# Kernel optimization log

Measured on AMD Instinct MI355X. Metric: run time of the kernel, lower is better.

## Reference

```python
import jax, jax.numpy as jnp
import numpy as np

L, B, T, D, H, F, V = 8, 2, 1024, 1024, 16, 4096, 50257


def _ln(x, w, b):
    m = jnp.mean(x, axis=-1, keepdims=True)
    v = jnp.mean((x - m) ** 2, axis=-1, keepdims=True)
    return (x - m) * jax.lax.rsqrt(v + 1e-5) * w + b


def setup_inputs() -> dict:
    key = jax.random.key(0)
    ks = iter(jax.random.split(key, 16))
    s = jnp.float32(0.02)
    w = lambda shape: jax.random.normal(next(ks), shape, jnp.float32) * s
    return {
        'idx': jax.random.randint(next(ks), (B, T), 0, V, jnp.int32),
        'emb': w((V, D)),
        'pos_emb': w((T, D)),
        'ln1_w': jnp.ones((L, D), jnp.float32),
        'ln1_b': jnp.zeros((L, D), jnp.float32),
        'qkv_w': w((L, D, 3 * D)),
        'qkv_b': jnp.zeros((L, 3 * D), jnp.float32),
        'ln2_w': jnp.ones((L, D), jnp.float32),
        'ln2_b': jnp.zeros((L, D), jnp.float32),
        'fc1_w': w((L, D, F)),
        'fc1_b': jnp.zeros((L, F), jnp.float32),
        'fc2_w': w((L, F, D)),
        'fc2_b': jnp.zeros((L, D), jnp.float32),
        'lnf_w': jnp.ones((D,), jnp.float32),
        'lnf_b': jnp.zeros((D,), jnp.float32),
        'head_w': w((D, V)),
        'head_b': jnp.zeros((V,), jnp.float32),
    }


def reference(idx, emb, pos_emb, ln1_w, ln1_b, qkv_w, qkv_b, ln2_w, ln2_b,
              fc1_w, fc1_b, fc2_w, fc2_b, lnf_w, lnf_b, head_w, head_b):
    b, t = idx.shape
    d = emb.shape[1]
    hd = d // H
    x = emb[idx] + pos_emb[:t]                      # [b,t,d]
    mask = jnp.tril(jnp.ones((t, t), bool))         # causal mask
    inv_scale = jnp.float32(1.0 / (d ** 0.5))       # NOTE: source scales by sqrt(full dim), not head_dim

    def layer(x, p):
        l1w, l1b, qw, qb, l2w, l2b, f1w, f1b, f2w, f2b = p
        h = _ln(x, l1w, l1b)
        qkv = h @ qw + qb                           # [b,t,3d]
        q, k, v = jnp.split(qkv, 3, axis=-1)
        q = q.reshape(b, t, H, hd)
        k = k.reshape(b, t, H, hd)
        v = v.reshape(b, t, H, hd)
        logits = jnp.einsum('bqhe,bkhe->bhqk', q, k) * inv_scale
        logits = jnp.where(mask, logits, -jnp.inf)
        attn = jax.nn.softmax(logits, axis=-1)
        o = jnp.einsum('bhqk,bkhe->bqhe', attn, v).reshape(b, t, d)
        x = x + o                                   # no output projection in source
        h = _ln(x, l2w, l2b)
        h = jax.nn.gelu(h @ f1w + f1b, approximate=False)
        h = jax.nn.gelu(h @ f2w + f2b, approximate=False)  # GELU after fc2 too, per source
        return x + h, None

    x, _ = jax.lax.scan(
        layer, x,
        (ln1_w, ln1_b, qkv_w, qkv_b, ln2_w, ln2_b, fc1_w, fc1_b, fc2_w, fc2_b))
    x = _ln(x, lnf_w, lnf_b)
    return x @ head_w + head_b                      # [b,t,V] logits
```

## Files before the change

kernel.cpp:

```cpp
#include <hip/hip_runtime.h>
#include <math.h>

#define Ln 8
#define Bn 2
#define Tn 1024
#define Dm 1024
#define Hn 16
#define Fm 4096
#define Vn 50257
#define NTOK 2048

typedef unsigned short u16;
typedef u16   u16x8  __attribute__((ext_vector_type(8)));
typedef __bf16 bf16x8 __attribute__((ext_vector_type(8)));
typedef float f32x4  __attribute__((ext_vector_type(4)));

__device__ __forceinline__ u16 f2bf(float f){
  unsigned u = __builtin_bit_cast(unsigned, f);
  u += 0x7FFFu + ((u >> 16) & 1u);
  return (u16)(u >> 16);
}
__device__ __forceinline__ float bf2f(u16 s){
  return __builtin_bit_cast(float, ((unsigned)s) << 16);
}
__device__ __forceinline__ float gelu_f(float v){
  return 0.5f * v * (1.0f + erff(v * 0.70710678118654752440f));
}
__device__ __forceinline__ void gload16(const void* g, void* l){
  __builtin_amdgcn_global_load_lds(
      (const __attribute__((address_space(1))) void*)g,
      (__attribute__((address_space(3))) void*)l, 16, 0, 0);
}

__global__ __launch_bounds__(256) void embed_kernel(const int* __restrict__ idx,
                                                    const float* __restrict__ emb,
                                                    const float* __restrict__ pos,
                                                    float* __restrict__ x){
  int row = blockIdx.x;
  int t = row & (Tn - 1);
  int id = idx[row];
  const float4* e = (const float4*)(emb + (size_t)id * Dm);
  const float4* p = (const float4*)(pos + (size_t)t * Dm);
  float4* o = (float4*)(x + (size_t)row * Dm);
  int i = threadIdx.x;
  float4 a = e[i], b = p[i];
  o[i] = make_float4(a.x + b.x, a.y + b.y, a.z + b.z, a.w + b.w);
}

__global__ __launch_bounds__(256) void ln_kernel(const float* __restrict__ xin,
                                                 const float* __restrict__ w,
                                                 const float* __restrict__ bb,
                                                 u16* __restrict__ out){
  int row = blockIdx.x;
  int t = threadIdx.x;
  float4 v = ((const float4*)(xin + (size_t)row * Dm))[t];
  float s  = v.x + v.y + v.z + v.w;
  float s2 = v.x*v.x + v.y*v.y + v.z*v.z + v.w*v.w;
  #pragma unroll
  for (int off = 1; off < 64; off <<= 1){
    s  += __shfl_xor(s, off);
    s2 += __shfl_xor(s2, off);
  }
  __shared__ float red[8];
  int wv = t >> 6, lane = t & 63;
  if (lane == 0){ red[wv] = s; red[4 + wv] = s2; }
  __syncthreads();
  s  = red[0] + red[1] + red[2] + red[3];
  s2 = red[4] + red[5] + red[6] + red[7];
  float mean = s * (1.0f / Dm);
  float var  = s2 * (1.0f / Dm) - mean * mean;
  float rs = rsqrtf(var + 1e-5f);
  float4 wv4 = ((const float4*)w)[t];
  float4 bv4 = ((const float4*)bb)[t];
  u16 o4[4];
  o4[0] = f2bf((v.x - mean) * rs * wv4.x + bv4.x);
  o4[1] = f2bf((v.y - mean) * rs * wv4.y + bv4.y);
  o4[2] = f2bf((v.z - mean) * rs * wv4.z + bv4.z);
  o4[3] = f2bf((v.w - mean) * rs * wv4.w + bv4.w);
  *(uint2*)(out + (size_t)row * Dm + t * 4) = *(uint2*)o4;
}

__device__ __forceinline__ void trans_tile(const float* __restrict__ src,
                                           u16* __restrict__ dst,
                                           int N, int K, int srcCol, int dstRow, int k0){
  __shared__ float tile[64][66];
  int t = threadIdx.x;
  int rr = t >> 4, nc = (t & 15) * 4;
  #pragma unroll
  for (int u = 0; u < 4; u++){
    int kk = rr + u * 16;
    int gn = srcCol + nc;
    const float* sp = src + (size_t)(k0 + kk) * N;
    float4 v;
    if (gn + 3 < N) v = *(const float4*)(sp + gn);
    else {
      v.x = (gn     < N) ? sp[gn]     : 0.0f;
      v.y = (gn + 1 < N) ? sp[gn + 1] : 0.0f;
      v.z = (gn + 2 < N) ? sp[gn + 2] : 0.0f;
      v.w = (gn + 3 < N) ? sp[gn + 3] : 0.0f;
    }
    tile[kk][nc]     = v.x;
    tile[kk][nc + 1] = v.y;
    tile[kk][nc + 2] = v.z;
    tile[kk][nc + 3] = v.w;
  }
  __syncthreads();
  int np = t >> 2, c = t & 3;
  u16* dp = dst + (size_t)(dstRow + np) * K + k0;
  u16 pk[8];
  #pragma unroll
  for (int j = 0; j < 8; j++) pk[j] = f2bf(tile[c*8 + j][np]);
  *(int4*)(dp + c*8) = *(int4*)pk;
  #pragma unroll
  for (int j = 0; j < 8; j++) pk[j] = f2bf(tile[32 + c*8 + j][np]);
  *(int4*)(dp + 32 + c*8) = *(int4*)pk;
}

__global__ __launch_bounds__(256) void transpose_w(const float* __restrict__ Bw,
                                                   u16* __restrict__ Bt,
                                                   int N, int K, int c0){
  int n0 = blockIdx.x * 64, k0 = blockIdx.y * 64;
  trans_tile(Bw, Bt, N, K, c0 + n0, n0, k0);
}

__global__ __launch_bounds__(256) void mega_transpose(const float* __restrict__ qkvw,
                                                      const float* __restrict__ fc1w,
                                                      const float* __restrict__ fc2w,
                                                      const float* __restrict__ headw,
                                                      u16* __restrict__ Wq,
                                                      u16* __restrict__ W1,
                                                      u16* __restrict__ W2,
                                                      u16* __restrict__ Wh){
  int id = blockIdx.x;
  const float* src; u16* dst; int N, K, n0, k0;
  if (id < 6144){
    int l = id / 768, r = id % 768;
    n0 = (r % 48) * 64; k0 = (r / 48) * 64;
    src = qkvw + (size_t)l * Dm * 3072; dst = Wq + (size_t)l * 3072 * Dm;
    N = 3072; K = Dm;
  } else if (id < 14336){
    int id2 = id - 6144;
    int l = id2 / 1024, r = id2 % 1024;
    n0 = (r % 64) * 64; k0 = (r / 64) * 64;
    src = fc1w + (size_t)l * Dm * Fm; dst = W1 + (size_t)l * Fm * Dm;
    N = Fm; K = Dm;
  } else if (id < 22528){
    int id2 = id - 14336;
    int l = id2 / 1024, r = id2 % 1024;
    n0 = (r % 16) * 64; k0 = (r / 16) * 64;
    src = fc2w + (size_t)l * Fm * Dm; dst = W2 + (size_t)l * Dm * Fm;
    N = Dm; K = Fm;
  } else {
    int id2 = id - 22528;
    n0 = (id2 % 788) * 64; k0 = (id2 / 788) * 64;
    src = headw; dst = Wh;
    N = Vn; K = Dm;
  }
  trans_tile(src, dst, N, K, n0, n0, k0);
}

template<int MODE, int BMt, int BNt, int WM, int WN, bool SWZ>
__global__ __launch_bounds__(256) void gemm_kernel(const u16* __restrict__ A,
                                                   const u16* __restrict__ Bt,
                                                   const float* __restrict__ bias,
                                                   void* __restrict__ outp,
                                                   float* __restrict__ resid,
                                                   u16* __restrict__ vT,
                                                   int K, int Nout, int c0){
  constexpr int MR = BMt / (WM * 16);
  constexpr int NR = BNt / (WN * 16);
  __shared__ u16 sA[BMt][64];
  __shared__ u16 sB[BNt][64];
  int t = threadIdx.x;
  int lane = t & 63, w = t >> 6;
  int wm = w / WN, wn = w % WN;
  int lr = lane & 15, lg = lane >> 4;
  int m0, n0;
  if (SWZ){
    int orig = blockIdx.x;
    int q = gridDim.x >> 3;
    int wg = (orig & 7) * q + (orig >> 3);
    m0 = (wg & 15) * BMt;
    n0 = (wg >> 4) * BNt;
  } else {
    m0 = blockIdx.y * BMt; n0 = blockIdx.x * BNt;
  }

  f32x4 acc[MR][NR] = {};

  int srow = lane >> 3;
  int gcs = ((lane & 7) ^ (lane >> 3)) * 8;
  int cswz = (lr & 7) << 3;

  for (int k0 = 0; k0 < K; k0 += 64){
    __syncthreads();
    #pragma unroll
    for (int i = 0; i < BMt/32; i++){
      int rbase = i*32 + w*8;
      gload16(A + (size_t)(m0 + rbase + srow) * K + k0 + gcs, (char*)&sA[rbase][0]);
    }
    #pragma unroll
    for (int i = 0; i < BNt/32; i++){
      int rbase = i*32 + w*8;
      gload16(Bt + (size_t)(n0 + rbase + srow) * K + k0 + gcs, (char*)&sB[rbase][0]);
    }
    __syncthreads();
    #pragma unroll
    for (int kk = 0; kk < 2; kk++){
      bf16x8 af[MR], bfr[NR];
      #pragma unroll
      for (int i = 0; i < MR; i++) af[i]  = *(const bf16x8*)&sA[wm*(MR*16) + i*16 + lr][(kk*32 + lg*8) ^ cswz];
      #pragma unroll
      for (int j = 0; j < NR; j++) bfr[j] = *(const bf16x8*)&sB[wn*(NR*16) + j*16 + lr][(kk*32 + lg*8) ^ cswz];
      #pragma unroll
      for (int i = 0; i < MR; i++)
        #pragma unroll
        for (int j = 0; j < NR; j++)
          acc[i][j] = __builtin_amdgcn_mfma_f32_16x16x32_bf16(af[i], bfr[j], acc[i][j], 0, 0, 0);
    }
  }

  #pragma unroll
  for (int i = 0; i < MR; i++){
    int gr0 = m0 + wm*(MR*16) + i*16 + lg*4;
    #pragma unroll
    for (int j = 0; j < NR; j++){
      int gc = c0 + n0 + wn*(NR*16) + j*16 + lr;
      if (MODE == 3 && gc >= Nout) continue;
      float bb = bias[gc];
      if (MODE == 0 && gc >= 2048){
        int hh = (gc - 2048) >> 6, dd = (gc - 2048) & 63;
        int b_ = gr0 >> 10, tt = gr0 & 1023;
        u16 pk[4];
        #pragma unroll
        for (int r = 0; r < 4; r++) pk[r] = f2bf(acc[i][j][r] + bb);
        *(uint2*)&vT[((size_t)((b_*Hn + hh)*64 + dd))*Tn + tt] = *(uint2*)pk;
        continue;
      }
      #pragma unroll
      for (int r = 0; r < 4; r++){
        float v = acc[i][j][r] + bb;
        size_t oi = (size_t)(gr0 + r) * Nout + gc;
        if (MODE == 0)      ((u16*)outp)[oi] = f2bf(v);
        else if (MODE == 1) ((u16*)outp)[oi] = f2bf(gelu_f(v));
        else if (MODE == 2) resid[oi] = resid[oi] + gelu_f(v);
        else                ((float*)outp)[oi] = v;
      }
    }
  }
}

#define BARR() __builtin_amdgcn_s_barrier()
#define LGK0() asm volatile("s_waitcnt lgkmcnt(0)" ::: "memory")
#define VMC4() asm volatile("s_waitcnt vmcnt(4)" ::: "memory")

__global__ __launch_bounds__(512) void head_gemm_8ph(const u16* __restrict__ A,
                                                     const u16* __restrict__ Bw,
                                                     const float* __restrict__ bias,
                                                     float* __restrict__ out){
  __shared__ u16 sA[2][256][64];
  __shared__ u16 sB[2][256][64];
  int t = threadIdx.x, lane = t & 63, w = t >> 6;
  int wm = w >> 2, wn = w & 3;
  int lr = lane & 15, lg = lane >> 4;
  int orig = blockIdx.x;
  int wg = (orig & 7) * (gridDim.x >> 3) + (orig >> 3);
  int m0g = (wg & 7) << 8;
  int n0g = (wg >> 3) << 8;

  int srow = w*8 + (lane >> 3);
  int scol = ((lane & 7) ^ (lane >> 3)) * 8;
  const u16* Abase = A  + (size_t)(m0g + srow) * 1024 + scol;
  const u16* Bbase = Bw + (size_t)(n0g + srow) * 1024 + scol;

  f32x4 acc[8][4] = {};
  bf16x8 a[4][2], b0[2][2], b1[2][2];
  int rsw = (lr & 7) << 3;

  auto stA = [&](int buf, int half, int tile){
    const u16* s = Abase + (size_t)half*128*1024 + tile*64;
    gload16(s,           &sA[buf][half*128 +      w*8][0]);
    gload16(s + 64*1024, &sA[buf][half*128 + 64 + w*8][0]);
  };
  auto stB = [&](int buf, int half, int tile){
    const u16* s = Bbase + (size_t)half*128*1024 + tile*64;
    gload16(s,           &sB[buf][half*128 +      w*8][0]);
    gload16(s + 64*1024, &sB[buf][half*128 + 64 + w*8][0]);
  };
  auto rdA = [&](int buf, int half){
    #pragma unroll
    for (int i = 0; i < 4; i++)
      #pragma unroll
      for (int kk = 0; kk < 2; kk++)
        a[i][kk] = *(const bf16x8*)&sA[buf][wm*128 + half*64 + i*16 + lr][(kk*32 + lg*8) ^ rsw];
  };
  auto rdB = [&](int buf, int half, bf16x8 (&bb)[2][2]){
    #pragma unroll
    for (int j = 0; j < 2; j++)
      #pragma unroll
      for (int kk = 0; kk < 2; kk++)
        bb[j][kk] = *(const bf16x8*)&sB[buf][wn*64 + half*32 + j*16 + lr][(kk*32 + lg*8) ^ rsw];
  };
  auto MF = [&](int mb, int nb, bf16x8 (&bb)[2][2]){
    __builtin_amdgcn_s_setprio(1);
    #pragma unroll
    for (int kk = 0; kk < 2; kk++)
      #pragma unroll
      for (int i = 0; i < 4; i++)
        #pragma unroll
        for (int j = 0; j < 2; j++)
          acc[mb+i][nb+j] = __builtin_amdgcn_mfma_f32_16x16x32_bf16(a[i][kk], bb[j][kk], acc[mb+i][nb+j], 0, 0, 0);
    __builtin_amdgcn_s_setprio(0);
  };

  stA(0,0,0); stA(0,1,0); stB(0,0,0); stB(0,1,0);
  stB(1,0,1); stB(1,1,1);
  VMC4();
  BARR();

  for (int it = 0; it < 8; ++it){
    int T = it * 2;
    rdA(0,0); rdB(0,0,b0);
    stA(1,0,T+1);
    BARR(); LGK0(); MF(0,0,b0); BARR();
    rdB(0,1,b1);
    stA(1,1,T+1);
    BARR(); LGK0(); MF(0,2,b1); BARR();
    rdA(0,1);
    if (T+2 < 16) stB(0,0,T+2);
    BARR(); LGK0(); MF(4,2,b1); BARR();
    if (T+2 < 16) stB(0,1,T+2);
    BARR(); MF(4,0,b0); VMC4(); BARR();
    rdA(1,0); rdB(1,0,b0);
    if (T+2 < 16) stA(0,0,T+2);
    BARR(); LGK0(); MF(0,0,b0); BARR();
    rdB(1,1,b1);
    if (T+2 < 16) stA(0,1,T+2);
    BARR(); LGK0(); MF(0,2,b1); BARR();
    rdA(1,1);
    if (T+3 < 16) stB(1,0,T+3);
    BARR(); LGK0(); MF(4,2,b1); BARR();
    if (T+3 < 16) stB(1,1,T+3);
    BARR(); MF(4,0,b0); VMC4(); BARR();
  }

  #pragma unroll
  for (int m = 0; m < 8; m++){
    int gr = m0g + wm*128 + m*16 + lg*4;
    #pragma unroll
    for (int n = 0; n < 4; n++){
      int gc = n0g + wn*64 + n*16 + lr;
      if (gc < Vn){
        float bb = bias[gc];
        #pragma unroll
        for (int r = 0; r < 4; r++)
          out[(size_t)(gr + r) * Vn + gc] = acc[m][n][r] + bb;
      }
    }
  }
}

__global__ __launch_bounds__(256) void attn_mfma(const u16* __restrict__ qkv,
                                                 const u16* __restrict__ vT,
                                                 float* __restrict__ x){
  int bid = blockIdx.x;
  int bh = bid & 31;
  int j = bid >> 5;
  int qt = (j < 8) ? (15 - j) : (j - 8);
  int b = bh >> 4, h_ = bh & 15;
  int t = threadIdx.x;
  int w = t >> 6, lane = t & 63;
  int lr = lane & 15, lg = lane >> 4;

  __shared__ u16 sK [2][64][72];
  __shared__ u16 sVt[2][64][72];
  __shared__ u16 sP [64][72];

  const u16* qbase = qkv + ((size_t)(b*Tn + qt*64 + w*16 + lr)) * 3*Dm + h_*64 + lg*8;
  bf16x8 qf[2];
  #pragma unroll
  for (int i = 0; i < 2; i++){
    u16x8 raw = *(const u16x8*)(qbase + i * 32);
    #pragma unroll
    for (int u = 0; u < 8; u++) qf[i][u] = (__bf16)(bf2f(raw[u]) * 0.03125f);
  }

  f32x4 o_[4] = {};
  float m_[4], l_[4];
  #pragma unroll
  for (int r = 0; r < 4; r++){ m_[r] = -INFINITY; l_[r] = 0.0f; }

  int sr = t >> 2, scc = (t & 3) * 16;
  const u16* kbase = qkv + ((size_t)(b*Tn + sr)) * 3*Dm + Dm + h_*64 + scc;
  const u16* vbase = vT + ((size_t)(bh*64 + sr)) * Tn + scc;
  int4 kr0, kr1, vr0, vr1;

  kr0 = *(const int4*)(kbase);     kr1 = *(const int4*)(kbase + 8);
  vr0 = *(const int4*)(vbase);     vr1 = *(const int4*)(vbase + 8);
  *(int4*)&sK [0][sr][scc]     = kr0;  *(int4*)&sK [0][sr][scc + 8] = kr1;
  *(int4*)&sVt[0][sr][scc]     = vr0;  *(int4*)&sVt[0][sr][scc + 8] = vr1;

  for (int kt = 0; kt <= qt; kt++){
    int cur = kt & 1;
    if (kt < qt){
      const u16* kb = kbase + (size_t)(kt + 1) * 64 * 3 * Dm;
      const u16* vb = vbase + (kt + 1) * 64;
      kr0 = *(const int4*)(kb);    kr1 = *(const int4*)(kb + 8);
      vr0 = *(const int4*)(vb);    vr1 = *(const int4*)(vb + 8);
    }
    __syncthreads();

    f32x4 s[4] = {};
    __builtin_amdgcn_s_setprio(1);
    #pragma unroll
    for (int kf = 0; kf < 2; kf++){
      #pragma unroll
      for (int nf = 0; nf < 4; nf++){
        bf16x8 kfrag = *(const bf16x8*)&sK[cur][nf*16 + lr][kf*32 + lg*8];
        s[nf] = __builtin_amdgcn_mfma_f32_16x16x32_bf16(qf[kf], kfrag, s[nf], 0, 0, 0);
      }
    }
    __builtin_amdgcn_s_setprio(0);

    bool lastt = (kt == qt);
    float tmax[4] = {-INFINITY, -INFINITY, -INFINITY, -INFINITY};
    #pragma unroll
    for (int nf = 0; nf < 4; nf++)
      #pragma unroll
      for (int r = 0; r < 4; r++){
        float v = s[nf][r];
        if (lastt){
          int kkg = nf*16 + lr, qg = w*16 + lg*4 + r;
          if (kkg > qg) v = -INFINITY;
        }
        s[nf][r] = v;
        tmax[r] = fmaxf(tmax[r], v);
      }
    #pragma unroll
    for (int r = 0; r < 4; r++){
      tmax[r] = fmaxf(tmax[r], __shfl_xor(tmax[r], 1));
      tmax[r] = fmaxf(tmax[r], __shfl_xor(tmax[r], 2));
      tmax[r] = fmaxf(tmax[r], __shfl_xor(tmax[r], 4));
      tmax[r] = fmaxf(tmax[r], __shfl_xor(tmax[r], 8));
    }
    bool need = false;
    #pragma unroll
    for (int r = 0; r < 4; r++) need = need || (tmax[r] > m_[r] + 8.0f);
    if (__any(need)){
      #pragma unroll
      for (int r = 0; r < 4; r++){
        float nm = fmaxf(m_[r], tmax[r]);
        float resc = __expf(m_[r] - nm);
        m_[r] = nm;
        l_[r] *= resc;
        #pragma unroll
        for (int df = 0; df < 4; df++) o_[df][r] *= resc;
      }
    }
    float psum[4] = {0.f, 0.f, 0.f, 0.f};
    #pragma unroll
    for (int nf = 0; nf < 4; nf++)
      #pragma unroll
      for (int r = 0; r < 4; r++){
        float pv = __expf(s[nf][r] - m_[r]);
        s[nf][r] = pv;
        psum[r] += pv;
      }
    #pragma unroll
    for (int r = 0; r < 4; r++){
      psum[r] += __shfl_xor(psum[r], 1);
      psum[r] += __shfl_xor(psum[r], 2);
      psum[r] += __shfl_xor(psum[r], 4);
      psum[r] += __shfl_xor(psum[r], 8);
      l_[r] += psum[r];
    }

    #pragma unroll
    for (int nf = 0; nf < 4; nf++)
      #pragma unroll
      for (int r = 0; r < 4; r++)
        sP[w*16 + lg*4 + r][nf*16 + lr] = f2bf(s[nf][r]);

    __builtin_amdgcn_s_setprio(1);
    #pragma unroll
    for (int kf = 0; kf < 2; kf++){
      bf16x8 pfrag = *(const bf16x8*)&sP[w*16 + lr][kf*32 + lg*8];
      #pragma unroll
      for (int df = 0; df < 4; df++){
        bf16x8 vfrag = *(const bf16x8*)&sVt[cur][df*16 + lr][kf*32 + lg*8];
        o_[df] = __builtin_amdgcn_mfma_f32_16x16x32_bf16(pfrag, vfrag, o_[df], 0, 0, 0);
      }
    }
    __builtin_amdgcn_s_setprio(0);

    if (kt < qt){
      int nxt = cur ^ 1;
      *(int4*)&sK [nxt][sr][scc]     = kr0;  *(int4*)&sK [nxt][sr][scc + 8] = kr1;
      *(int4*)&sVt[nxt][sr][scc]     = vr0;  *(int4*)&sVt[nxt][sr][scc + 8] = vr1;
    }
  }

  float inv[4];
  #pragma unroll
  for (int r = 0; r < 4; r++) inv[r] = 1.0f / l_[r];
  #pragma unroll
  for (int df = 0; df < 4; df++)
    #pragma unroll
    for (int r = 0; r < 4; r++){
      float* xr = x + ((size_t)(b*Tn + qt*64 + w*16 + lg*4 + r)) * Dm + h_*64 + df*16 + lr;
      *xr += o_[df][r] * inv[r];
    }
}

extern "C" void kernel_launch(void* const* d_in, const int* in_sizes, int n_in,
                              void* d_out, int out_size, void* d_ws, size_t ws_size,
                              hipStream_t stream){
  const int*   idx   = (const int*)  d_in[0];
  const float* emb   = (const float*)d_in[1];
  const float* pos   = (const float*)d_in[2];
  const float* ln1w  = (const float*)d_in[3];
  const float* ln1b  = (const float*)d_in[4];
  const float* qkvw  = (const float*)d_in[5];
  const float* qkvb  = (const float*)d_in[6];
  const float* ln2w  = (const float*)d_in[7];
  const float* ln2b  = (const float*)d_in[8];
  const float* fc1w  = (const float*)d_in[9];
  const float* fc1b  = (const float*)d_in[10];
  const float* fc2w  = (const float*)d_in[11];
  const float* fc2b  = (const float*)d_in[12];
  const float* lnfw  = (const float*)d_in[13];
  const float* lnfb  = (const float*)d_in[14];
  const float* headw = (const float*)d_in[15];
  const float* headb = (const float*)d_in[16];
  float* out = (float*)d_out;

  const size_t MB = 1u << 20;
  char* ws = (char*)d_ws;
  float* x   = (float*)(ws);
  u16*   h   = (u16*)  (ws + 8*MB);
  u16*   qkv = (u16*)  (ws + 12*MB);
  u16*   f1  = (u16*)  (ws + 24*MB);

  bool mega    = ws_size >= 320*MB;
  bool bighead = ws_size >= 116*MB;

  u16 *vT, *Bt = nullptr, *BtF = nullptr, *Wq = nullptr, *W1 = nullptr, *W2 = nullptr, *Wh = nullptr;
  if (mega){
    vT = (u16*)(ws + 40*MB);
    Wq = (u16*)(ws + 44*MB);
    W1 = (u16*)(ws + 92*MB);
    W2 = (u16*)(ws + 156*MB);
    Wh = (u16*)(ws + 220*MB);
  } else {
    Bt  = (u16*)(ws + 40*MB);
    vT  = (u16*)(ws + 48*MB);
    BtF = (u16*)(ws + 12*MB);
  }

  if (mega)
    mega_transpose<<<35136, 256, 0, stream>>>(qkvw, fc1w, fc2w, headw, Wq, W1, W2, Wh);

  embed_kernel<<<NTOK, 256, 0, stream>>>(idx, emb, pos, x);

  for (int l = 0; l < Ln; l++){
    const u16* Bq = mega ? Wq + (size_t)l*3072*Dm : Bt;
    const u16* B1 = mega ? W1 + (size_t)l*Fm*Dm   : Bt;
    const u16* B2 = mega ? W2 + (size_t)l*Dm*Fm   : Bt;
    ln_kernel<<<NTOK, 256, 0, stream>>>(x, ln1w + l*Dm, ln1b + l*Dm, h);
    if (!mega) transpose_w<<<dim3(3072/64, Dm/64), 256, 0, stream>>>(qkvw + (size_t)l*Dm*3072, Bt, 3072, Dm, 0);
    gemm_kernel<0, 64,128,1,4,false><<<dim3(3072/128, NTOK/64), 256, 0, stream>>>(h, Bq, qkvb + l*3072, qkv, nullptr, vT, Dm, 3072, 0);
    attn_mfma<<<512, 256, 0, stream>>>(qkv, vT, x);
    ln_kernel<<<NTOK, 256, 0, stream>>>(x, ln2w + l*Dm, ln2b + l*Dm, h);
    if (!mega) transpose_w<<<dim3(Fm/64, Dm/64), 256, 0, stream>>>(fc1w + (size_t)l*Dm*Fm, Bt, Fm, Dm, 0);
    gemm_kernel<1,128,128,2,2,false><<<dim3(Fm/128, NTOK/128), 256, 0, stream>>>(h, B1, fc1b + l*Fm, f1, nullptr, nullptr, Dm, Fm, 0);
    if (!mega) transpose_w<<<dim3(Dm/64, Fm/64), 256, 0, stream>>>(fc2w + (size_t)l*Fm*Dm, Bt, Dm, Fm, 0);
    gemm_kernel<2, 64,64,2,2,false><<<dim3(Dm/64, NTOK/64), 256, 0, stream>>>(f1, B2, fc2b + l*Dm, nullptr, x, nullptr, Fm, Dm, 0);
  }

  ln_kernel<<<NTOK, 256, 0, stream>>>(x, lnfw, lnfb, h);

  if (mega){
    head_gemm_8ph<<<1576, 512, 0, stream>>>(h, Wh, headb, out);
  } else if (bighead){
    transpose_w<<<dim3(786, Dm/64), 256, 0, stream>>>(headw, BtF, Vn, Dm, 0);
    gemm_kernel<3,128,128,2,2,true><<<6288, 256, 0, stream>>>(h, BtF, headb, out, nullptr, nullptr, Dm, Vn, 0);
  } else {
    const int CHUNK = 4096;
    for (int c0 = 0; c0 < Vn; c0 += CHUNK){
      int W = Vn - c0; if (W > CHUNK) W = CHUNK;
      int ngx = (W + 127) / 128;
      transpose_w<<<dim3(ngx * 2, Dm/64), 256, 0, stream>>>(headw, Bt, Vn, Dm, c0);
      gemm_kernel<3,128,128,2,2,false><<<dim3(ngx, NTOK/128), 256, 0, stream>>>(h, Bt, headb, out, nullptr, nullptr, Dm, Vn, c0);
    }
  }
}
```

Before: 1.735 ms.

## Fuse LayerNorm apply into QKV and FC1 GEMM A-tile loads

Replaces the per-layer LayerNorm kernels that wrote a bf16 normalized copy with a small stats kernel (mean, rstd per row) plus normalization applied on the fly while staging A tiles in the QKV and FC1 GEMMs. This removes the bf16 h write and reread per LN. In exchange, each GEMM block re-reads the fp32 activations (twice the bytes of bf16) for every N tile and loses the async global-to-LDS load path for A, doing the normalize/convert in registers. Variance is now computed as E[x^2]-mean^2, which is slightly less numerically stable.

```diff
diff --git a/kernel.cpp b/kernel.cpp
--- a/kernel.cpp
+++ b/kernel.cpp
@@ -45,6 +45,30 @@
   int i = threadIdx.x;
   float4 a = e[i], b = p[i];
   o[i] = make_float4(a.x + b.x, a.y + b.y, a.z + b.z, a.w + b.w);
+}
+
+__global__ __launch_bounds__(256) void ln_stats(const float* __restrict__ xin,
+                                                float2* __restrict__ st){
+  int row = blockIdx.x * 4 + (threadIdx.x >> 6);
+  int lane = threadIdx.x & 63;
+  const float4* xr = (const float4*)(xin + (size_t)row * Dm);
+  float s = 0.0f, s2 = 0.0f;
+  #pragma unroll
+  for (int i = 0; i < 4; i++){
+    float4 v = xr[lane + i * 64];
+    s  += v.x + v.y + v.z + v.w;
+    s2 += v.x*v.x + v.y*v.y + v.z*v.z + v.w*v.w;
+  }
+  #pragma unroll
+  for (int off = 1; off < 64; off <<= 1){
+    s  += __shfl_xor(s, off);
+    s2 += __shfl_xor(s2, off);
+  }
+  if (lane == 0){
+    float mean = s * (1.0f / Dm);
+    float var  = s2 * (1.0f / Dm) - mean * mean;
+    st[row] = make_float2(mean, rsqrtf(var + 1e-5f));
+  }
 }
 
 __global__ __launch_bounds__(256) void ln_kernel(const float* __restrict__ xin,
@@ -159,16 +183,22 @@
   trans_tile(src, dst, N, K, n0, n0, k0);
 }
 
-template<int MODE, int BMt, int BNt, int WM, int WN, bool SWZ>
+template<int MODE, int BMt, int BNt, int WM, int WN, bool SWZ, bool FUSE>
 __global__ __launch_bounds__(256) void gemm_kernel(const u16* __restrict__ A,
                                                    const u16* __restrict__ Bt,
                                                    const float* __restrict__ bias,
                                                    void* __restrict__ outp,
                                                    float* __restrict__ resid,
                                                    u16* __restrict__ vT,
+                                                   const float* __restrict__ xin,
+                                                   const float2* __restrict__ stats,
+                                                   const float* __restrict__ lnw,
+                                                   const float* __restrict__ lnb,
                                                    int K, int Nout, int c0){
   constexpr int MR = BMt / (WM * 16);
   constexpr int NR = BNt / (WN * 16);
+  constexpr int TPR = 256 / BMt;
+  constexpr int CPT = 64 / TPR;
   __shared__ u16 sA[BMt][64];
   __shared__ u16 sB[BNt][64];
   int t = threadIdx.x;
@@ -192,12 +222,35 @@
   int gcs = ((lane & 7) ^ (lane >> 3)) * 8;
   int cswz = (lr & 7) << 3;
 
+  int frow = t / TPR;
+  int fcl  = (t % TPR) * CPT;
+  float2 mr = FUSE ? stats[m0 + frow] : make_float2(0.f, 0.f);
+  const float* xrow = FUSE ? (xin + (size_t)(m0 + frow) * 1024 + fcl) : nullptr;
+
   for (int k0 = 0; k0 < K; k0 += 64){
     __syncthreads();
-    #pragma unroll
-    for (int i = 0; i < BMt/32; i++){
-      int rbase = i*32 + w*8;
-      gload16(A + (size_t)(m0 + rbase + srow) * K + k0 + gcs, (char*)&sA[rbase][0]);
+    if (FUSE){
+      u16 pk[CPT];
+      #pragma unroll
+      for (int ci = 0; ci < CPT; ci += 4){
+        float4 v  = *(const float4*)(xrow + k0 + ci);
+        float4 wv = *(const float4*)(lnw + k0 + fcl + ci);
+        float4 bv = *(const float4*)(lnb + k0 + fcl + ci);
+        pk[ci+0] = f2bf((v.x - mr.x) * mr.y * wv.x + bv.x);
+        pk[ci+1] = f2bf((v.y - mr.x) * mr.y * wv.y + bv.y);
+        pk[ci+2] = f2bf((v.z - mr.x) * mr.y * wv.z + bv.z);
+        pk[ci+3] = f2bf((v.w - mr.x) * mr.y * wv.w + bv.w);
+      }
+      int s0 = fcl >> 3;
+      #pragma unroll
+      for (int sj = 0; sj < CPT/8; sj++)
+        *(int4*)&sA[frow][((s0 + sj) ^ (frow & 7)) * 8] = *(int4*)&pk[sj*8];
+    } else {
+      #pragma unroll
+      for (int i = 0; i < BMt/32; i++){
+        int rbase = i*32 + w*8;
+        gload16(A + (size_t)(m0 + rbase + srow) * K + k0 + gcs, (char*)&sA[rbase][0]);
+      }
     }
     #pragma unroll
     for (int i = 0; i < BNt/32; i++){
@@ -536,24 +589,25 @@
 
   const size_t MB = 1u << 20;
   char* ws = (char*)d_ws;
-  float* x   = (float*)(ws);
-  u16*   h   = (u16*)  (ws + 8*MB);
-  u16*   qkv = (u16*)  (ws + 12*MB);
-  u16*   f1  = (u16*)  (ws + 24*MB);
+  float*  x     = (float*)(ws);
+  u16*    h     = (u16*)  (ws + 8*MB);
+  u16*    qkv   = (u16*)  (ws + 12*MB);
+  u16*    f1    = (u16*)  (ws + 24*MB);
+  float2* stats = (float2*)(ws + 40*MB);
 
   bool mega    = ws_size >= 320*MB;
   bool bighead = ws_size >= 116*MB;
 
   u16 *vT, *Bt = nullptr, *BtF = nullptr, *Wq = nullptr, *W1 = nullptr, *W2 = nullptr, *Wh = nullptr;
   if (mega){
-    vT = (u16*)(ws + 40*MB);
-    Wq = (u16*)(ws + 44*MB);
-    W1 = (u16*)(ws + 92*MB);
-    W2 = (u16*)(ws + 156*MB);
-    Wh = (u16*)(ws + 220*MB);
+    vT = (u16*)(ws + 41*MB);
+    Wq = (u16*)(ws + 45*MB);
+    W1 = (u16*)(ws + 93*MB);
+    W2 = (u16*)(ws + 157*MB);
+    Wh = (u16*)(ws + 221*MB);
   } else {
-    Bt  = (u16*)(ws + 40*MB);
-    vT  = (u16*)(ws + 48*MB);
+    Bt  = (u16*)(ws + 41*MB);
+    vT  = (u16*)(ws + 49*MB);
     BtF = (u16*)(ws + 12*MB);
   }
 
@@ -566,15 +620,18 @@
     const u16* Bq = mega ? Wq + (size_t)l*3072*Dm : Bt;
     const u16* B1 = mega ? W1 + (size_t)l*Fm*Dm   : Bt;
     const u16* B2 = mega ? W2 + (size_t)l*Dm*Fm   : Bt;
-    ln_kernel<<<NTOK, 256, 0, stream>>>(x, ln1w + l*Dm, ln1b + l*Dm, h);
+    ln_stats<<<NTOK/4, 256, 0, stream>>>(x, stats);
     if (!mega) transpose_w<<<dim3(3072/64, Dm/64), 256, 0, stream>>>(qkvw + (size_t)l*Dm*3072, Bt, 3072, Dm, 0);
-    gemm_kernel<0, 64,128,1,4,false><<<dim3(3072/128, NTOK/64), 256, 0, stream>>>(h, Bq, qkvb + l*3072, qkv, nullptr, vT, Dm, 3072, 0);
+    gemm_kernel<0, 64,128,1,4,false,true><<<dim3(3072/128, NTOK/64), 256, 0, stream>>>(
+        nullptr, Bq, qkvb + l*3072, qkv, nullptr, vT, x, stats, ln1w + l*Dm, ln1b + l*Dm, Dm, 3072, 0);
     attn_mfma<<<512, 256, 0, stream>>>(qkv, vT, x);
-    ln_kernel<<<NTOK, 256, 0, stream>>>(x, ln2w + l*Dm, ln2b + l*Dm, h);
+    ln_stats<<<NTOK/4, 256, 0, stream>>>(x, stats);
     if (!mega) transpose_w<<<dim3(Fm/64, Dm/64), 256, 0, stream>>>(fc1w + (size_t)l*Dm*Fm, Bt, Fm, Dm, 0);
-    gemm_kernel<1,128,128,2,2,false><<<dim3(Fm/128, NTOK/128), 256, 0, stream>>>(h, B1, fc1b + l*Fm, f1, nullptr, nullptr, Dm, Fm, 0);
+    gemm_kernel<1,128,128,2,2,false,true><<<dim3(Fm/128, NTOK/128), 256, 0, stream>>>(
+        nullptr, B1, fc1b + l*Fm, f1, nullptr, nullptr, x, stats, ln2w + l*Dm, ln2b + l*Dm, Dm, Fm, 0);
     if (!mega) transpose_w<<<dim3(Dm/64, Fm/64), 256, 0, stream>>>(fc2w + (size_t)l*Fm*Dm, Bt, Dm, Fm, 0);
-    gemm_kernel<2, 64,64,2,2,false><<<dim3(Dm/64, NTOK/64), 256, 0, stream>>>(f1, B2, fc2b + l*Dm, nullptr, x, nullptr, Fm, Dm, 0);
+    gemm_kernel<2, 64,64,2,2,false,false><<<dim3(Dm/64, NTOK/64), 256, 0, stream>>>(
+        f1, B2, fc2b + l*Dm, nullptr, x, nullptr, nullptr, nullptr, nullptr, nullptr, Fm, Dm, 0);
   }
 
   ln_kernel<<<NTOK, 256, 0, stream>>>(x, lnfw, lnfb, h);
@@ -583,14 +640,16 @@
     head_gemm_8ph<<<1576, 512, 0, stream>>>(h, Wh, headb, out);
   } else if (bighead){
     transpose_w<<<dim3(786, Dm/64), 256, 0, stream>>>(headw, BtF, Vn, Dm, 0);
-    gemm_kernel<3,128,128,2,2,true><<<6288, 256, 0, stream>>>(h, BtF, headb, out, nullptr, nullptr, Dm, Vn, 0);
+    gemm_kernel<3,128,128,2,2,true,false><<<6288, 256, 0, stream>>>(
+        h, BtF, headb, out, nullptr, nullptr, nullptr, nullptr, nullptr, nullptr, Dm, Vn, 0);
   } else {
     const int CHUNK = 4096;
     for (int c0 = 0; c0 < Vn; c0 += CHUNK){
       int W = Vn - c0; if (W > CHUNK) W = CHUNK;
       int ngx = (W + 127) / 128;
       transpose_w<<<dim3(ngx * 2, Dm/64), 256, 0, stream>>>(headw, Bt, Vn, Dm, c0);
-      gemm_kernel<3,128,128,2,2,false><<<dim3(ngx, NTOK/128), 256, 0, stream>>>(h, Bt, headb, out, nullptr, nullptr, Dm, Vn, c0);
-    }
-  }
-}
+      gemm_kernel<3,128,128,2,2,false,false><<<dim3(ngx, NTOK/128), 256, 0, stream>>>(
+          h, Bt, headb, out, nullptr, nullptr, nullptr, nullptr, nullptr, nullptr, Dm, Vn, c0);
+    }
+  }
+}
```

After: 2.348 ms. 35.4% more time.
